# Optimization experiments

Hardware: AMD Instinct MI355X
Metric: run time of the kernel (lower is better)

The kernel has to match this reference:

```python
import jax, jax.numpy as jnp
import numpy as np

D_MODEL = 1024
NUM_HEADS = 16
HEAD_DIM = D_MODEL // NUM_HEADS

def setup_inputs() -> dict:
    key = jax.random.key(0)
    ks = jax.random.split(key, 9)
    B, L = 2, 2048
    s = 1.0 / np.sqrt(D_MODEL)
    return {
        "x":  jax.random.normal(ks[0], (B, L, D_MODEL), dtype=jnp.float32),
        "Wq": jax.random.uniform(ks[1], (D_MODEL, D_MODEL), jnp.float32, -s, s),
        "bq": jax.random.uniform(ks[2], (D_MODEL,), jnp.float32, -s, s),
        "Wk": jax.random.uniform(ks[3], (D_MODEL, D_MODEL), jnp.float32, -s, s),
        "bk": jax.random.uniform(ks[4], (D_MODEL,), jnp.float32, -s, s),
        "Wv": jax.random.uniform(ks[5], (D_MODEL, D_MODEL), jnp.float32, -s, s),
        "bv": jax.random.uniform(ks[6], (D_MODEL,), jnp.float32, -s, s),
        "Wo": jax.random.uniform(ks[7], (D_MODEL, D_MODEL), jnp.float32, -s, s),
        "bo": jax.random.uniform(ks[8], (D_MODEL,), jnp.float32, -s, s),
    }

def _split_heads(t):
    B, L, _ = t.shape
    return t.reshape(B, L, NUM_HEADS, HEAD_DIM).transpose(0, 2, 1, 3)  # [B,H,L,Dh]

def reference(x, Wq, bq, Wk, bk, Wv, bv, Wo, bo):
    # Linear projections (torch Linear: y = x @ W.T + b)
    Q = _split_heads(x @ Wq.T + bq)
    K = _split_heads(x @ Wk.T + bk)
    V = _split_heads(x @ Wv.T + bv)
    scale = 1.0 / jnp.sqrt(jnp.asarray(HEAD_DIM, dtype=x.dtype))
    scores = jnp.einsum('bhqd,bhkd->bhqk', Q, K) * scale  # [B,H,L,L]
    attn_weights = jax.nn.softmax(scores, axis=-1)
    ctx = jnp.einsum('bhqk,bhkd->bhqd', attn_weights, V)  # [B,H,L,Dh]
    B, H, L, Dh = ctx.shape
    ctx = ctx.transpose(0, 2, 1, 3).reshape(B, L, H * Dh)
    out = ctx @ Wo.T + bo  # dropout p=0.0 -> identity
    return (out, attn_weights)
```

## Files before the change

### kernel.cpp

```cpp
#include <hip/hip_runtime.h>

typedef unsigned short u16;
typedef __bf16 bf16x8 __attribute__((ext_vector_type(8)));
typedef float f32x4 __attribute__((ext_vector_type(4)));

#define WSTR 72

__device__ __forceinline__ u16 f2bf(float f) {
    union { float f; unsigned int u; } v; v.f = f;
    unsigned int u = v.u;
    u += 0x7fffu + ((u >> 16) & 1u);
    return (u16)(u >> 16);
}

__device__ __forceinline__ u16 cvt_bf(float f) {
    __bf16 h = (__bf16)f;
    union { __bf16 h; u16 u; } v; v.h = h; return v.u;
}

__device__ __forceinline__ void gload16(const u16* g, u16* l) {
    __builtin_amdgcn_global_load_lds((const __attribute__((address_space(1))) unsigned int*)(const void*)g,
                                     (__attribute__((address_space(3))) unsigned int*)(void*)l, 16, 0, 0);
}

__global__ __launch_bounds__(256) void k_cvtX(const float* __restrict__ src, u16* __restrict__ dst) {
    const size_t i = ((size_t)blockIdx.x * 256 + threadIdx.x) * 8;
    float4 v0 = *(const float4*)(src + i);
    float4 v1 = *(const float4*)(src + i + 4);
    u16 o[8];
    o[0] = f2bf(v0.x); o[1] = f2bf(v0.y); o[2] = f2bf(v0.z); o[3] = f2bf(v0.w);
    o[4] = f2bf(v1.x); o[5] = f2bf(v1.y); o[6] = f2bf(v1.z); o[7] = f2bf(v1.w);
    *(uint4*)(dst + i) = *(const uint4*)o;
}

__global__ __launch_bounds__(256) void k_cvtW(const float* __restrict__ w0, const float* __restrict__ w1,
                                              const float* __restrict__ w2, const float* __restrict__ w3,
                                              u16* __restrict__ dst) {
    const int z = blockIdx.z;
    const float* src = z == 0 ? w0 : z == 1 ? w1 : z == 2 ? w2 : w3;
    const size_t i = ((size_t)blockIdx.x * 256 + threadIdx.x) * 8;
    float4 v0 = *(const float4*)(src + i);
    float4 v1 = *(const float4*)(src + i + 4);
    u16 o[8];
    o[0] = f2bf(v0.x); o[1] = f2bf(v0.y); o[2] = f2bf(v0.z); o[3] = f2bf(v0.w);
    o[4] = f2bf(v1.x); o[5] = f2bf(v1.y); o[6] = f2bf(v1.z); o[7] = f2bf(v1.w);
    *(uint4*)(dst + (size_t)z * 1048576 + i) = *(const uint4*)o;
}

__global__ __launch_bounds__(256) void k_qkv(const u16* __restrict__ Xb, const u16* __restrict__ Wb,
                                             const float* __restrict__ bq, const float* __restrict__ bk,
                                             const float* __restrict__ bv,
                                             u16* __restrict__ Q, u16* __restrict__ Kd, u16* __restrict__ Vt) {
    __shared__ __align__(16) u16 lA[128 * 32];
    __shared__ __align__(16) u16 lB[128 * 32];
    const int t = threadIdx.x;
    const int n0 = blockIdx.x * 128;
    const int m0 = blockIdx.y * 128;
    const int lane = t & 63, wave = t >> 6;
    const int wm = (wave >> 1) * 64, wn = (wave & 1) * 64;
    const int quad = lane >> 4, m16 = lane & 15;
    const int r4 = t >> 2, c8 = (t & 3) * 8;
    f32x4 acc[4][4] = {};
    for (int k0 = 0; k0 < 1024; k0 += 32) {
        gload16(Xb + (size_t)(m0 + r4) * 1024 + k0 + c8,       &lA[t * 8]);
        gload16(Xb + (size_t)(m0 + 64 + r4) * 1024 + k0 + c8,  &lA[2048 + t * 8]);
        gload16(Wb + (size_t)(n0 + r4) * 1024 + k0 + c8,       &lB[t * 8]);
        gload16(Wb + (size_t)(n0 + 64 + r4) * 1024 + k0 + c8,  &lB[2048 + t * 8]);
        __syncthreads();
        bf16x8 af[4], bfr[4];
#pragma unroll
        for (int i = 0; i < 4; ++i) {
            af[i]  = *(const bf16x8*)(lA + (wm + i * 16 + m16) * 32 + quad * 8);
            bfr[i] = *(const bf16x8*)(lB + (wn + i * 16 + m16) * 32 + quad * 8);
        }
#pragma unroll
        for (int mi = 0; mi < 4; ++mi)
#pragma unroll
            for (int ni = 0; ni < 4; ++ni)
                acc[mi][ni] = __builtin_amdgcn_mfma_f32_16x16x32_bf16(af[mi], bfr[ni], acc[mi][ni], 0, 0, 0);
        __syncthreads();
    }
#pragma unroll
    for (int ni = 0; ni < 4; ++ni) {
        const int gcol = n0 + wn + ni * 16 + m16;
        const int mat = gcol >> 10;
        const int col = gcol & 1023;
        const int h = col >> 6, d = col & 63;
        const float bias = (mat == 0 ? bq : mat == 1 ? bk : bv)[col];
        u16* dst = mat == 0 ? Q : mat == 1 ? Kd : Vt;
#pragma unroll
        for (int mi = 0; mi < 4; ++mi)
#pragma unroll
            for (int e = 0; e < 4; ++e) {
                const int row = m0 + wm + mi * 16 + quad * 4 + e;
                const int b = row >> 11, l = row & 2047;
                const float v = acc[mi][ni][e] + bias;
                size_t idx;
                if (mat == 2) idx = (((size_t)(b * 16 + h)) * 64 + d) * 2048 + l;
                else          idx = (((size_t)(b * 16 + h)) * 2048 + l) * 64 + d;
                dst[idx] = cvt_bf(v);
            }
    }
}

#define MFMA16(A, B, C) __builtin_amdgcn_mfma_f32_16x16x32_bf16(A, B, C, 0, 0, 0)

__global__ __launch_bounds__(256) void k_attn(const u16* __restrict__ Q,
                                              const u16* __restrict__ K,
                                              const u16* __restrict__ Vt,
                                              float* __restrict__ attn,
                                              u16* __restrict__ ctx) {
    __shared__ __align__(16) u16 lW[2 * 64 * WSTR];
    __shared__ float sred[2][64];
    const int t = threadIdx.x;
    const int bh = blockIdx.y;
    const int m0 = blockIdx.x * 64;
    const int lane = t & 63, wave = t >> 6;
    const int wq = (wave & 1) * 32;
    const int wk = (wave >> 1) * 32;
    const int wm = (wave >> 1) * 32, wn = (wave & 1) * 32;
    const int quad = lane >> 4, m16 = lane & 15;
    const u16* Qh = Q + (size_t)bh * 2048 * 64;
    const u16* Kh = K + (size_t)bh * 2048 * 64;
    const u16* Vh = Vt + (size_t)bh * 64 * 2048;
    float* ah = attn + ((size_t)bh << 22) + (size_t)m0 * 2048;

    const float SC = 0.18033688011112042f;

    bf16x8 qf[2][2];
#pragma unroll
    for (int ni = 0; ni < 2; ++ni)
#pragma unroll
        for (int ks = 0; ks < 2; ++ks)
            qf[ni][ks] = *(const bf16x8*)(Qh + (size_t)(m0 + wq + ni * 16 + m16) * 64 + ks * 32 + quad * 8);

    const u16* kpl = Kh + (size_t)(wk + m16) * 64 + quad * 8;
    const u16* vpl = Vh + (size_t)(wn + m16) * 2048 + quad * 8;

    float slane[2] = {0.f, 0.f};
    {
        bf16x8 k00 = *(const bf16x8*)(kpl);
        bf16x8 k01 = *(const bf16x8*)(kpl + 32);
        bf16x8 k10 = *(const bf16x8*)(kpl + 1024);
        bf16x8 k11 = *(const bf16x8*)(kpl + 1024 + 32);
        for (int kt = 0; kt < 32; ++kt) {
            const u16* nx = kpl + (size_t)(kt + 1) * 4096;
            bf16x8 n00 = *(const bf16x8*)(nx);
            bf16x8 n01 = *(const bf16x8*)(nx + 32);
            bf16x8 n10 = *(const bf16x8*)(nx + 1024);
            bf16x8 n11 = *(const bf16x8*)(nx + 1024 + 32);
            f32x4 sacc[2][2] = {};
            sacc[0][0] = MFMA16(k00, qf[0][0], sacc[0][0]);
            sacc[0][1] = MFMA16(k00, qf[1][0], sacc[0][1]);
            sacc[1][0] = MFMA16(k10, qf[0][0], sacc[1][0]);
            sacc[1][1] = MFMA16(k10, qf[1][0], sacc[1][1]);
            sacc[0][0] = MFMA16(k01, qf[0][1], sacc[0][0]);
            sacc[0][1] = MFMA16(k01, qf[1][1], sacc[0][1]);
            sacc[1][0] = MFMA16(k11, qf[0][1], sacc[1][0]);
            sacc[1][1] = MFMA16(k11, qf[1][1], sacc[1][1]);
#pragma unroll
            for (int mi = 0; mi < 2; ++mi)
#pragma unroll
                for (int e = 0; e < 4; ++e) {
                    slane[0] += __builtin_amdgcn_exp2f(sacc[mi][0][e] * SC);
                    slane[1] += __builtin_amdgcn_exp2f(sacc[mi][1][e] * SC);
                }
            k00 = n00; k01 = n01; k10 = n10; k11 = n11;
        }
    }
#pragma unroll
    for (int ni = 0; ni < 2; ++ni) {
        slane[ni] += __shfl_xor(slane[ni], 16);
        slane[ni] += __shfl_xor(slane[ni], 32);
    }
    if (quad == 0) {
        sred[wave >> 1][wq + m16]      = slane[0];
        sred[wave >> 1][wq + 16 + m16] = slane[1];
    }
    __syncthreads();
    float inv[2];
    inv[0] = 1.0f / (sred[0][wq + m16]      + sred[1][wq + m16]);
    inv[1] = 1.0f / (sred[0][wq + 16 + m16] + sred[1][wq + 16 + m16]);

    unsigned aoff[2][2], lwoff[2][2];
#pragma unroll
    for (int mi = 0; mi < 2; ++mi)
#pragma unroll
        for (int ni = 0; ni < 2; ++ni) {
            const int q = wq + ni * 16 + m16;
            const int k = wk + mi * 16 + quad * 4;
            aoff[mi][ni]  = (unsigned)(q * 2048 + k);
            lwoff[mi][ni] = (unsigned)(q * WSTR + k);
        }

    f32x4 cacc[2][2] = {};
    {
        bf16x8 k00 = *(const bf16x8*)(kpl);
        bf16x8 k01 = *(const bf16x8*)(kpl + 32);
        bf16x8 k10 = *(const bf16x8*)(kpl + 1024);
        bf16x8 k11 = *(const bf16x8*)(kpl + 1024 + 32);
        int buf = 0;
        for (int kt = 0; kt < 32; ++kt) {
            const u16* nx = kpl + (size_t)(kt + 1) * 4096;
            bf16x8 n00 = *(const bf16x8*)(nx);
            bf16x8 n01 = *(const bf16x8*)(nx + 32);
            bf16x8 n10 = *(const bf16x8*)(nx + 1024);
            bf16x8 n11 = *(const bf16x8*)(nx + 1024 + 32);
            f32x4 sacc[2][2] = {};
            sacc[0][0] = MFMA16(k00, qf[0][0], sacc[0][0]);
            sacc[0][1] = MFMA16(k00, qf[1][0], sacc[0][1]);
            sacc[1][0] = MFMA16(k10, qf[0][0], sacc[1][0]);
            sacc[1][1] = MFMA16(k10, qf[1][0], sacc[1][1]);
            sacc[0][0] = MFMA16(k01, qf[0][1], sacc[0][0]);
            sacc[0][1] = MFMA16(k01, qf[1][1], sacc[0][1]);
            sacc[1][0] = MFMA16(k11, qf[0][1], sacc[1][0]);
            sacc[1][1] = MFMA16(k11, qf[1][1], sacc[1][1]);
#pragma unroll
            for (int mi = 0; mi < 2; ++mi)
#pragma unroll
                for (int ni = 0; ni < 2; ++ni)
#pragma unroll
                    for (int e = 0; e < 4; ++e)
                        sacc[mi][ni][e] = __builtin_amdgcn_exp2f(sacc[mi][ni][e] * SC) * inv[ni];
            bf16x8 v00 = *(const bf16x8*)(vpl + kt * 64);
            bf16x8 v01 = *(const bf16x8*)(vpl + kt * 64 + 32);
            bf16x8 v10 = *(const bf16x8*)(vpl + 32768 + kt * 64);
            bf16x8 v11 = *(const bf16x8*)(vpl + 32768 + kt * 64 + 32);
            u16* lwb = lW + buf * (64 * WSTR);
#pragma unroll
            for (int mi = 0; mi < 2; ++mi)
#pragma unroll
                for (int ni = 0; ni < 2; ++ni) {
                    u16 p[4];
                    p[0] = cvt_bf(sacc[mi][ni][0]); p[1] = cvt_bf(sacc[mi][ni][1]);
                    p[2] = cvt_bf(sacc[mi][ni][2]); p[3] = cvt_bf(sacc[mi][ni][3]);
                    *(uint2*)&lwb[lwoff[mi][ni]] = *(const uint2*)p;
                }
            __syncthreads();
            float* ap = ah + kt * 64;
#pragma unroll
            for (int mi = 0; mi < 2; ++mi)
#pragma unroll
                for (int ni = 0; ni < 2; ++ni)
                    *(f32x4*)(ap + aoff[mi][ni]) = sacc[mi][ni];
            bf16x8 a00 = *(const bf16x8*)(lwb + (wm + m16) * WSTR + quad * 8);
            bf16x8 a01 = *(const bf16x8*)(lwb + (wm + m16) * WSTR + 32 + quad * 8);
            bf16x8 a10 = *(const bf16x8*)(lwb + (wm + 16 + m16) * WSTR + quad * 8);
            bf16x8 a11 = *(const bf16x8*)(lwb + (wm + 16 + m16) * WSTR + 32 + quad * 8);
            cacc[0][0] = MFMA16(a00, v00, cacc[0][0]);
            cacc[0][1] = MFMA16(a00, v10, cacc[0][1]);
            cacc[1][0] = MFMA16(a10, v00, cacc[1][0]);
            cacc[1][1] = MFMA16(a10, v10, cacc[1][1]);
            cacc[0][0] = MFMA16(a01, v01, cacc[0][0]);
            cacc[0][1] = MFMA16(a01, v11, cacc[0][1]);
            cacc[1][0] = MFMA16(a11, v01, cacc[1][0]);
            cacc[1][1] = MFMA16(a11, v11, cacc[1][1]);
            k00 = n00; k01 = n01; k10 = n10; k11 = n11;
            buf ^= 1;
        }
    }

    const int b = bh >> 4, h = bh & 15;
    u16* cp = ctx + ((size_t)b * 2048) * 1024 + h * 64;
#pragma unroll
    for (int mi = 0; mi < 2; ++mi)
#pragma unroll
        for (int ni = 0; ni < 2; ++ni)
#pragma unroll
            for (int e = 0; e < 4; ++e) {
                const int row = m0 + wm + mi * 16 + quad * 4 + e;
                const int col = wn + ni * 16 + m16;
                cp[(size_t)row * 1024 + col] = cvt_bf(cacc[mi][ni][e]);
            }
}

__global__ __launch_bounds__(256) void k_out(const u16* __restrict__ ctx,
                                             const u16* __restrict__ WoB,
                                             const float* __restrict__ bo,
                                             float* __restrict__ out) {
    __shared__ __align__(16) u16 lA[128 * 32];
    __shared__ __align__(16) u16 lB[128 * 32];
    const int t = threadIdx.x;
    const int n0 = blockIdx.x * 128;
    const int m0 = blockIdx.y * 128;
    const int lane = t & 63, wave = t >> 6;
    const int wm = (wave >> 1) * 64, wn = (wave & 1) * 64;
    const int quad = lane >> 4, m16 = lane & 15;
    const int r4 = t >> 2, c8 = (t & 3) * 8;
    f32x4 acc[4][4] = {};
    for (int k0 = 0; k0 < 1024; k0 += 32) {
        gload16(ctx + (size_t)(m0 + r4) * 1024 + k0 + c8,       &lA[t * 8]);
        gload16(ctx + (size_t)(m0 + 64 + r4) * 1024 + k0 + c8,  &lA[2048 + t * 8]);
        gload16(WoB + (size_t)(n0 + r4) * 1024 + k0 + c8,       &lB[t * 8]);
        gload16(WoB + (size_t)(n0 + 64 + r4) * 1024 + k0 + c8,  &lB[2048 + t * 8]);
        __syncthreads();
        bf16x8 af[4], bfr[4];
#pragma unroll
        for (int i = 0; i < 4; ++i) {
            af[i]  = *(const bf16x8*)(lA + (wm + i * 16 + m16) * 32 + quad * 8);
            bfr[i] = *(const bf16x8*)(lB + (wn + i * 16 + m16) * 32 + quad * 8);
        }
#pragma unroll
        for (int mi = 0; mi < 4; ++mi)
#pragma unroll
            for (int ni = 0; ni < 4; ++ni)
                acc[mi][ni] = __builtin_amdgcn_mfma_f32_16x16x32_bf16(af[mi], bfr[ni], acc[mi][ni], 0, 0, 0);
        __syncthreads();
    }
#pragma unroll
    for (int ni = 0; ni < 4; ++ni) {
        const int col = n0 + wn + ni * 16 + m16;
        const float bv = bo[col];
#pragma unroll
        for (int mi = 0; mi < 4; ++mi)
#pragma unroll
            for (int e = 0; e < 4; ++e) {
                const int row = m0 + wm + mi * 16 + quad * 4 + e;
                out[(size_t)row * 1024 + col] = acc[mi][ni][e] + bv;
            }
    }
}

extern "C" void kernel_launch(void* const* d_in, const int* in_sizes, int n_in,
                              void* d_out, int out_size, void* d_ws, size_t ws_size,
                              hipStream_t stream) {
    const float* x  = (const float*)d_in[0];
    const float* Wq = (const float*)d_in[1];
    const float* bq = (const float*)d_in[2];
    const float* Wk = (const float*)d_in[3];
    const float* bk = (const float*)d_in[4];
    const float* Wv = (const float*)d_in[5];
    const float* bv = (const float*)d_in[6];
    const float* Wo = (const float*)d_in[7];
    const float* bo = (const float*)d_in[8];

    float* out_f = (float*)d_out;
    float* attn  = out_f + (size_t)4096 * 1024;

    u16* Xb = (u16*)d_ws;
    u16* Wb = Xb + (size_t)4194304;
    u16* Qb = Wb + (size_t)4194304;
    u16* Kb = Qb + (size_t)4194304;
    u16* Vt = Kb + (size_t)4194304;

    dim3 blk(256);
    k_cvtX<<<dim3(2048), blk, 0, stream>>>(x, Xb);
    k_cvtW<<<dim3(512, 1, 4), blk, 0, stream>>>(Wq, Wk, Wv, Wo, Wb);
    k_qkv<<<dim3(24, 32), blk, 0, stream>>>(Xb, Wb, bq, bk, bv, Qb, Kb, Vt);
    k_attn<<<dim3(32, 32), blk, 0, stream>>>(Qb, Kb, Vt, attn, Xb);
    k_out<<<dim3(8, 32), blk, 0, stream>>>(Xb, Wb + (size_t)3072 * 1024, bo, out_f);
}
```

Before: 845.4 us.

## Stage K/V tiles in LDS, add V transpose kernel, software-pipeline attention PV

The QKV GEMM now writes V in row-major layout to a scratch area borrowed from the attention output buffer, and a new k_vtr kernel transposes it through LDS. The old direct transposed store used strided 2-byte writes. In the attention kernel, K and V tiles are double-buffered in shared memory with one shared global load per block, replacing per-wave direct global fragment loads. The P·V MFMA is deferred by one iteration so the barrier before reading the probability tile overlaps with the next step. The grid is also swapped so blocks of the same head are adjacent, which should improve K/V cache reuse. This adds an extra kernel launch, more LDS per block and a barrier every iteration.

```diff
diff --git a/kernel.cpp b/kernel.cpp
--- a/kernel.cpp
+++ b/kernel.cpp
@@ -5,6 +5,7 @@
 typedef float f32x4 __attribute__((ext_vector_type(4)));
 
 #define WSTR 72
+#define TSZ (64 * WSTR)
 
 __device__ __forceinline__ u16 f2bf(float f) {
     union { float f; unsigned int u; } v; v.f = f;
@@ -22,6 +23,8 @@
     __builtin_amdgcn_global_load_lds((const __attribute__((address_space(1))) unsigned int*)(const void*)g,
                                      (__attribute__((address_space(3))) unsigned int*)(void*)l, 16, 0, 0);
 }
+
+#define MFMA16(A, B, C) __builtin_amdgcn_mfma_f32_16x16x32_bf16(A, B, C, 0, 0, 0)
 
 __global__ __launch_bounds__(256) void k_cvtX(const float* __restrict__ src, u16* __restrict__ dst) {
     const size_t i = ((size_t)blockIdx.x * 256 + threadIdx.x) * 8;
@@ -50,7 +53,7 @@
 __global__ __launch_bounds__(256) void k_qkv(const u16* __restrict__ Xb, const u16* __restrict__ Wb,
                                              const float* __restrict__ bq, const float* __restrict__ bk,
                                              const float* __restrict__ bv,
-                                             u16* __restrict__ Q, u16* __restrict__ Kd, u16* __restrict__ Vt) {
+                                             u16* __restrict__ Q, u16* __restrict__ Kd, u16* __restrict__ Vtmp) {
     __shared__ __align__(16) u16 lA[128 * 32];
     __shared__ __align__(16) u16 lB[128 * 32];
     const int t = threadIdx.x;
@@ -77,7 +80,7 @@
         for (int mi = 0; mi < 4; ++mi)
 #pragma unroll
             for (int ni = 0; ni < 4; ++ni)
-                acc[mi][ni] = __builtin_amdgcn_mfma_f32_16x16x32_bf16(af[mi], bfr[ni], acc[mi][ni], 0, 0, 0);
+                acc[mi][ni] = MFMA16(af[mi], bfr[ni], acc[mi][ni]);
         __syncthreads();
     }
 #pragma unroll
@@ -87,39 +90,57 @@
         const int col = gcol & 1023;
         const int h = col >> 6, d = col & 63;
         const float bias = (mat == 0 ? bq : mat == 1 ? bk : bv)[col];
-        u16* dst = mat == 0 ? Q : mat == 1 ? Kd : Vt;
+        u16* dst = mat == 0 ? Q : mat == 1 ? Kd : Vtmp;
 #pragma unroll
         for (int mi = 0; mi < 4; ++mi)
 #pragma unroll
             for (int e = 0; e < 4; ++e) {
                 const int row = m0 + wm + mi * 16 + quad * 4 + e;
                 const int b = row >> 11, l = row & 2047;
-                const float v = acc[mi][ni][e] + bias;
-                size_t idx;
-                if (mat == 2) idx = (((size_t)(b * 16 + h)) * 64 + d) * 2048 + l;
-                else          idx = (((size_t)(b * 16 + h)) * 2048 + l) * 64 + d;
-                dst[idx] = cvt_bf(v);
-            }
-    }
-}
-
-#define MFMA16(A, B, C) __builtin_amdgcn_mfma_f32_16x16x32_bf16(A, B, C, 0, 0, 0)
+                dst[(((size_t)(b * 16 + h)) * 2048 + l) * 64 + d] = cvt_bf(acc[mi][ni][e] + bias);
+            }
+    }
+}
+
+__global__ __launch_bounds__(256) void k_vtr(const u16* __restrict__ Vtmp, u16* __restrict__ Vt) {
+    __shared__ __align__(16) u16 ld[64 * WSTR];
+    const int t = threadIdx.x;
+    const int bh = blockIdx.y;
+    const int l0 = blockIdx.x * 64;
+    const int r = t >> 3, c8 = (t & 7) * 8;
+    const u16* src = Vtmp + (size_t)bh * 2048 * 64 + (size_t)l0 * 64;
+    *(uint4*)&ld[r * WSTR + c8]        = *(const uint4*)(src + (size_t)r * 64 + c8);
+    *(uint4*)&ld[(r + 32) * WSTR + c8] = *(const uint4*)(src + (size_t)(r + 32) * 64 + c8);
+    __syncthreads();
+    u16* dst = Vt + (size_t)bh * 64 * 2048 + l0;
+#pragma unroll
+    for (int half = 0; half < 2; ++half) {
+        const int d = r + half * 32;
+        u16 p[8];
+#pragma unroll
+        for (int i = 0; i < 8; ++i) p[i] = ld[(c8 + i) * WSTR + d];
+        *(uint4*)(dst + (size_t)d * 2048 + c8) = *(const uint4*)p;
+    }
+}
 
 __global__ __launch_bounds__(256) void k_attn(const u16* __restrict__ Q,
                                               const u16* __restrict__ K,
                                               const u16* __restrict__ Vt,
                                               float* __restrict__ attn,
                                               u16* __restrict__ ctx) {
-    __shared__ __align__(16) u16 lW[2 * 64 * WSTR];
+    __shared__ __align__(16) u16 lK[2 * TSZ];
+    __shared__ __align__(16) u16 lV[2 * TSZ];
+    __shared__ __align__(16) u16 lW[2 * TSZ];
     __shared__ float sred[2][64];
     const int t = threadIdx.x;
-    const int bh = blockIdx.y;
-    const int m0 = blockIdx.x * 64;
+    const int bh = blockIdx.x;
+    const int m0 = blockIdx.y * 64;
     const int lane = t & 63, wave = t >> 6;
     const int wq = (wave & 1) * 32;
     const int wk = (wave >> 1) * 32;
     const int wm = (wave >> 1) * 32, wn = (wave & 1) * 32;
     const int quad = lane >> 4, m16 = lane & 15;
+    const int sr = t >> 3, sc = (t & 7) * 8;
     const u16* Qh = Q + (size_t)bh * 2048 * 64;
     const u16* Kh = K + (size_t)bh * 2048 * 64;
     const u16* Vh = Vt + (size_t)bh * 64 * 2048;
@@ -134,21 +155,24 @@
         for (int ks = 0; ks < 2; ++ks)
             qf[ni][ks] = *(const bf16x8*)(Qh + (size_t)(m0 + wq + ni * 16 + m16) * 64 + ks * 32 + quad * 8);
 
-    const u16* kpl = Kh + (size_t)(wk + m16) * 64 + quad * 8;
-    const u16* vpl = Vh + (size_t)(wn + m16) * 2048 + quad * 8;
-
     float slane[2] = {0.f, 0.f};
     {
-        bf16x8 k00 = *(const bf16x8*)(kpl);
-        bf16x8 k01 = *(const bf16x8*)(kpl + 32);
-        bf16x8 k10 = *(const bf16x8*)(kpl + 1024);
-        bf16x8 k11 = *(const bf16x8*)(kpl + 1024 + 32);
+        *(uint4*)&lK[sr * WSTR + sc]        = *(const uint4*)(Kh + (size_t)sr * 64 + sc);
+        *(uint4*)&lK[(sr + 32) * WSTR + sc] = *(const uint4*)(Kh + (size_t)(sr + 32) * 64 + sc);
+        int buf = 0;
         for (int kt = 0; kt < 32; ++kt) {
-            const u16* nx = kpl + (size_t)(kt + 1) * 4096;
-            bf16x8 n00 = *(const bf16x8*)(nx);
-            bf16x8 n01 = *(const bf16x8*)(nx + 32);
-            bf16x8 n10 = *(const bf16x8*)(nx + 1024);
-            bf16x8 n11 = *(const bf16x8*)(nx + 1024 + 32);
+            __syncthreads();
+            if (kt < 31) {
+                const u16* kp = Kh + (size_t)(kt + 1) * 64 * 64;
+                u16* dK = &lK[(buf ^ 1) * TSZ];
+                *(uint4*)&dK[sr * WSTR + sc]        = *(const uint4*)(kp + (size_t)sr * 64 + sc);
+                *(uint4*)&dK[(sr + 32) * WSTR + sc] = *(const uint4*)(kp + (size_t)(sr + 32) * 64 + sc);
+            }
+            const u16* lKb = &lK[buf * TSZ];
+            bf16x8 k00 = *(const bf16x8*)(lKb + (wk + m16) * WSTR + quad * 8);
+            bf16x8 k01 = *(const bf16x8*)(lKb + (wk + m16) * WSTR + 32 + quad * 8);
+            bf16x8 k10 = *(const bf16x8*)(lKb + (wk + 16 + m16) * WSTR + quad * 8);
+            bf16x8 k11 = *(const bf16x8*)(lKb + (wk + 16 + m16) * WSTR + 32 + quad * 8);
             f32x4 sacc[2][2] = {};
             sacc[0][0] = MFMA16(k00, qf[0][0], sacc[0][0]);
             sacc[0][1] = MFMA16(k00, qf[1][0], sacc[0][1]);
@@ -165,7 +189,7 @@
                     slane[0] += __builtin_amdgcn_exp2f(sacc[mi][0][e] * SC);
                     slane[1] += __builtin_amdgcn_exp2f(sacc[mi][1][e] * SC);
                 }
-            k00 = n00; k01 = n01; k10 = n10; k11 = n11;
+            buf ^= 1;
         }
     }
 #pragma unroll
@@ -194,18 +218,25 @@
         }
 
     f32x4 cacc[2][2] = {};
+    bf16x8 vp00 = {}, vp01 = {}, vp10 = {}, vp11 = {};
     {
-        bf16x8 k00 = *(const bf16x8*)(kpl);
-        bf16x8 k01 = *(const bf16x8*)(kpl + 32);
-        bf16x8 k10 = *(const bf16x8*)(kpl + 1024);
-        bf16x8 k11 = *(const bf16x8*)(kpl + 1024 + 32);
+        *(uint4*)&lK[sr * WSTR + sc]        = *(const uint4*)(Kh + (size_t)sr * 64 + sc);
+        *(uint4*)&lK[(sr + 32) * WSTR + sc] = *(const uint4*)(Kh + (size_t)(sr + 32) * 64 + sc);
+        *(uint4*)&lV[sr * WSTR + sc]        = *(const uint4*)(Vh + (size_t)sr * 2048 + sc);
+        *(uint4*)&lV[(sr + 32) * WSTR + sc] = *(const uint4*)(Vh + (size_t)(sr + 32) * 2048 + sc);
         int buf = 0;
         for (int kt = 0; kt < 32; ++kt) {
-            const u16* nx = kpl + (size_t)(kt + 1) * 4096;
-            bf16x8 n00 = *(const bf16x8*)(nx);
-            bf16x8 n01 = *(const bf16x8*)(nx + 32);
-            bf16x8 n10 = *(const bf16x8*)(nx + 1024);
-            bf16x8 n11 = *(const bf16x8*)(nx + 1024 + 32);
+            __syncthreads();
+            const u16* lKb = &lK[buf * TSZ];
+            const u16* lVb = &lV[buf * TSZ];
+            bf16x8 vn00 = *(const bf16x8*)(lVb + (wn + m16) * WSTR + quad * 8);
+            bf16x8 vn01 = *(const bf16x8*)(lVb + (wn + m16) * WSTR + 32 + quad * 8);
+            bf16x8 vn10 = *(const bf16x8*)(lVb + (wn + 16 + m16) * WSTR + quad * 8);
+            bf16x8 vn11 = *(const bf16x8*)(lVb + (wn + 16 + m16) * WSTR + 32 + quad * 8);
+            bf16x8 k00 = *(const bf16x8*)(lKb + (wk + m16) * WSTR + quad * 8);
+            bf16x8 k01 = *(const bf16x8*)(lKb + (wk + m16) * WSTR + 32 + quad * 8);
+            bf16x8 k10 = *(const bf16x8*)(lKb + (wk + 16 + m16) * WSTR + quad * 8);
+            bf16x8 k11 = *(const bf16x8*)(lKb + (wk + 16 + m16) * WSTR + 32 + quad * 8);
             f32x4 sacc[2][2] = {};
             sacc[0][0] = MFMA16(k00, qf[0][0], sacc[0][0]);
             sacc[0][1] = MFMA16(k00, qf[1][0], sacc[0][1]);
@@ -215,6 +246,16 @@
             sacc[0][1] = MFMA16(k01, qf[1][1], sacc[0][1]);
             sacc[1][0] = MFMA16(k11, qf[0][1], sacc[1][0]);
             sacc[1][1] = MFMA16(k11, qf[1][1], sacc[1][1]);
+            if (kt < 31) {
+                const u16* kp = Kh + (size_t)(kt + 1) * 64 * 64;
+                const u16* vp = Vh + (size_t)(kt + 1) * 64;
+                u16* dK = &lK[(buf ^ 1) * TSZ];
+                u16* dV = &lV[(buf ^ 1) * TSZ];
+                *(uint4*)&dK[sr * WSTR + sc]        = *(const uint4*)(kp + (size_t)sr * 64 + sc);
+                *(uint4*)&dK[(sr + 32) * WSTR + sc] = *(const uint4*)(kp + (size_t)(sr + 32) * 64 + sc);
+                *(uint4*)&dV[sr * WSTR + sc]        = *(const uint4*)(vp + (size_t)sr * 2048 + sc);
+                *(uint4*)&dV[(sr + 32) * WSTR + sc] = *(const uint4*)(vp + (size_t)(sr + 32) * 2048 + sc);
+            }
 #pragma unroll
             for (int mi = 0; mi < 2; ++mi)
 #pragma unroll
@@ -222,11 +263,7 @@
 #pragma unroll
                     for (int e = 0; e < 4; ++e)
                         sacc[mi][ni][e] = __builtin_amdgcn_exp2f(sacc[mi][ni][e] * SC) * inv[ni];
-            bf16x8 v00 = *(const bf16x8*)(vpl + kt * 64);
-            bf16x8 v01 = *(const bf16x8*)(vpl + kt * 64 + 32);
-            bf16x8 v10 = *(const bf16x8*)(vpl + 32768 + kt * 64);
-            bf16x8 v11 = *(const bf16x8*)(vpl + 32768 + kt * 64 + 32);
-            u16* lwb = lW + buf * (64 * WSTR);
+            u16* lwb = &lW[(kt & 1) * TSZ];
 #pragma unroll
             for (int mi = 0; mi < 2; ++mi)
 #pragma unroll
@@ -236,28 +273,44 @@
                     p[2] = cvt_bf(sacc[mi][ni][2]); p[3] = cvt_bf(sacc[mi][ni][3]);
                     *(uint2*)&lwb[lwoff[mi][ni]] = *(const uint2*)p;
                 }
-            __syncthreads();
             float* ap = ah + kt * 64;
 #pragma unroll
             for (int mi = 0; mi < 2; ++mi)
 #pragma unroll
                 for (int ni = 0; ni < 2; ++ni)
                     *(f32x4*)(ap + aoff[mi][ni]) = sacc[mi][ni];
-            bf16x8 a00 = *(const bf16x8*)(lwb + (wm + m16) * WSTR + quad * 8);
-            bf16x8 a01 = *(const bf16x8*)(lwb + (wm + m16) * WSTR + 32 + quad * 8);
-            bf16x8 a10 = *(const bf16x8*)(lwb + (wm + 16 + m16) * WSTR + quad * 8);
-            bf16x8 a11 = *(const bf16x8*)(lwb + (wm + 16 + m16) * WSTR + 32 + quad * 8);
-            cacc[0][0] = MFMA16(a00, v00, cacc[0][0]);
-            cacc[0][1] = MFMA16(a00, v10, cacc[0][1]);
-            cacc[1][0] = MFMA16(a10, v00, cacc[1][0]);
-            cacc[1][1] = MFMA16(a10, v10, cacc[1][1]);
-            cacc[0][0] = MFMA16(a01, v01, cacc[0][0]);
-            cacc[0][1] = MFMA16(a01, v11, cacc[0][1]);
-            cacc[1][0] = MFMA16(a11, v01, cacc[1][0]);
-            cacc[1][1] = MFMA16(a11, v11, cacc[1][1]);
-            k00 = n00; k01 = n01; k10 = n10; k11 = n11;
+            if (kt > 0) {
+                const u16* lwp = &lW[((kt - 1) & 1) * TSZ];
+                bf16x8 a00 = *(const bf16x8*)(lwp + (wm + m16) * WSTR + quad * 8);
+                bf16x8 a01 = *(const bf16x8*)(lwp + (wm + m16) * WSTR + 32 + quad * 8);
+                bf16x8 a10 = *(const bf16x8*)(lwp + (wm + 16 + m16) * WSTR + quad * 8);
+                bf16x8 a11 = *(const bf16x8*)(lwp + (wm + 16 + m16) * WSTR + 32 + quad * 8);
+                cacc[0][0] = MFMA16(a00, vp00, cacc[0][0]);
+                cacc[0][1] = MFMA16(a00, vp10, cacc[0][1]);
+                cacc[1][0] = MFMA16(a10, vp00, cacc[1][0]);
+                cacc[1][1] = MFMA16(a10, vp10, cacc[1][1]);
+                cacc[0][0] = MFMA16(a01, vp01, cacc[0][0]);
+                cacc[0][1] = MFMA16(a01, vp11, cacc[0][1]);
+                cacc[1][0] = MFMA16(a11, vp01, cacc[1][0]);
+                cacc[1][1] = MFMA16(a11, vp11, cacc[1][1]);
+            }
+            vp00 = vn00; vp01 = vn01; vp10 = vn10; vp11 = vn11;
             buf ^= 1;
         }
+        __syncthreads();
+        const u16* lwp = &lW[(31 & 1) * TSZ];
+        bf16x8 a00 = *(const bf16x8*)(lwp + (wm + m16) * WSTR + quad * 8);
+        bf16x8 a01 = *(const bf16x8*)(lwp + (wm + m16) * WSTR + 32 + quad * 8);
+        bf16x8 a10 = *(const bf16x8*)(lwp + (wm + 16 + m16) * WSTR + quad * 8);
+        bf16x8 a11 = *(const bf16x8*)(lwp + (wm + 16 + m16) * WSTR + 32 + quad * 8);
+        cacc[0][0] = MFMA16(a00, vp00, cacc[0][0]);
+        cacc[0][1] = MFMA16(a00, vp10, cacc[0][1]);
+        cacc[1][0] = MFMA16(a10, vp00, cacc[1][0]);
+        cacc[1][1] = MFMA16(a10, vp10, cacc[1][1]);
+        cacc[0][0] = MFMA16(a01, vp01, cacc[0][0]);
+        cacc[0][1] = MFMA16(a01, vp11, cacc[0][1]);
+        cacc[1][0] = MFMA16(a11, vp01, cacc[1][0]);
+        cacc[1][1] = MFMA16(a11, vp11, cacc[1][1]);
     }
 
     const int b = bh >> 4, h = bh & 15;
@@ -304,7 +357,7 @@
         for (int mi = 0; mi < 4; ++mi)
 #pragma unroll
             for (int ni = 0; ni < 4; ++ni)
-                acc[mi][ni] = __builtin_amdgcn_mfma_f32_16x16x32_bf16(af[mi], bfr[ni], acc[mi][ni], 0, 0, 0);
+                acc[mi][ni] = MFMA16(af[mi], bfr[ni], acc[mi][ni]);
         __syncthreads();
     }
 #pragma unroll
@@ -342,11 +395,13 @@
     u16* Qb = Wb + (size_t)4194304;
     u16* Kb = Qb + (size_t)4194304;
     u16* Vt = Kb + (size_t)4194304;
+    u16* Vtmp = (u16*)attn;
 
     dim3 blk(256);
     k_cvtX<<<dim3(2048), blk, 0, stream>>>(x, Xb);
     k_cvtW<<<dim3(512, 1, 4), blk, 0, stream>>>(Wq, Wk, Wv, Wo, Wb);
-    k_qkv<<<dim3(24, 32), blk, 0, stream>>>(Xb, Wb, bq, bk, bv, Qb, Kb, Vt);
+    k_qkv<<<dim3(24, 32), blk, 0, stream>>>(Xb, Wb, bq, bk, bv, Qb, Kb, Vtmp);
+    k_vtr<<<dim3(32, 32), blk, 0, stream>>>(Vtmp, Vt);
     k_attn<<<dim3(32, 32), blk, 0, stream>>>(Qb, Kb, Vt, attn, Xb);
     k_out<<<dim3(8, 32), blk, 0, stream>>>(Xb, Wb + (size_t)3072 * 1024, bo, out_f);
 }
```

Result: faster. 703.0 us (-16.8%).
